# Optimization experiments

Hardware: AMD Instinct MI355X
Metric: run time of the kernel (lower is better)

The kernel has to match this reference:

```python
import jax, jax.numpy as jnp
import numpy as np

EMBED_DIM = 1024
PROJ_DIM = 256


def setup_inputs() -> dict:
    key = jax.random.key(0)
    kx, kq, kk = jax.random.split(key, 3)
    x = jax.random.normal(kx, (8, 4096, EMBED_DIM), dtype=jnp.float32)
    scale = 1.0 / (PROJ_DIM ** 0.5)
    q_proj = jax.random.normal(kq, (EMBED_DIM, PROJ_DIM), dtype=jnp.float32) * scale
    k_proj = jax.random.normal(kk, (EMBED_DIM, PROJ_DIM), dtype=jnp.float32) * scale
    return {"x": x, "q_proj": q_proj, "k_proj": k_proj}


def reference(x, q_proj, k_proj):
    # exp feature maps (FAVOR-style)
    q_prime = jnp.exp(jnp.einsum('bld,de->ble', x, q_proj))  # [B, L, E]
    k_prime = jnp.exp(jnp.einsum('bld,de->ble', x, k_proj))  # [B, L, E]
    # associative KV summary: O(L*E*D)
    kv = jnp.einsum('ble,bld->bed', k_prime, x)               # [B, E, D]
    num = jnp.einsum('ble,bed->bld', q_prime, kv)             # [B, L, D]
    z = 1.0 / (jnp.sum(q_prime, axis=-1, keepdims=True) + 1e-8)
    return num * z
```

## Files before the change

### kernel.cpp

```cpp
#include <hip/hip_runtime.h>


#define EMBED 1024
#define PROJ  256
#define LSEQ  4096
#define BATCH 8

typedef short  bfrag __attribute__((ext_vector_type(8)));
typedef float  f4    __attribute__((ext_vector_type(4)));
typedef unsigned short u16x8 __attribute__((ext_vector_type(8)));
typedef unsigned short u16x4 __attribute__((ext_vector_type(4)));

static __device__ __forceinline__ unsigned short f2bf(float f) {
  unsigned int u = __builtin_bit_cast(unsigned int, f);
  u += 0x7fffu + ((u >> 16) & 1u);
  return (unsigned short)(u >> 16);
}
static __device__ __forceinline__ float bf2f(unsigned short h) {
  unsigned int u = ((unsigned int)h) << 16;
  return __builtin_bit_cast(float, u);
}

static __device__ __forceinline__ void gload_lds16(const void* g, void* l) {
  __builtin_amdgcn_global_load_lds(
      (__attribute__((address_space(1))) void*)(unsigned long long)(g),
      (__attribute__((address_space(3))) void*)(unsigned)(unsigned long long)(l),
      16, 0, 0);
}

static __device__ __forceinline__ void stage_tile(
    const unsigned short* __restrict__ src, int row0, int stride, int k0,
    unsigned short* lds, int wave, int lane) {
#pragma unroll
  for (int j = 0; j < 4; j++) {
    int slot = (wave * 4 + j) * 64 + lane;
    int r = slot >> 3, cp = slot & 7;
    int c = cp ^ (r & 7);
    gload_lds16(src + (size_t)(row0 + r) * stride + k0 + c * 8,
                lds + (wave * 4 + j) * 512);
  }
}

static __device__ __forceinline__ bfrag read_frag(const unsigned short* lds,
                                                  int row, int chunk) {
  return *(const bfrag*)(lds + ((row << 3) + (chunk ^ (row & 7))) * 8);
}

__global__ __launch_bounds__(256) void cvtx_kernel(
    const float* __restrict__ x, unsigned short* __restrict__ xb,
    unsigned short* __restrict__ xT) {
  __shared__ unsigned short T[64][72];
  const int tid = threadIdx.x;
  const int d0 = blockIdx.x * 64, l0 = blockIdx.y * 64, b = blockIdx.z;
#pragma unroll
  for (int it = 0; it < 4; it++) {
    int slot = it * 256 + tid;
    int r = slot >> 4, c4 = slot & 15;
    f4 v = *(const f4*)(x + ((size_t)(b * LSEQ + l0 + r)) * EMBED + d0 + c4 * 4);
    u16x4 h = (u16x4){f2bf(v[0]), f2bf(v[1]), f2bf(v[2]), f2bf(v[3])};
    *(u16x4*)(xb + ((size_t)(b * LSEQ + l0 + r)) * EMBED + d0 + c4 * 4) = h;
    T[c4 * 4 + 0][r] = h[0];
    T[c4 * 4 + 1][r] = h[1];
    T[c4 * 4 + 2][r] = h[2];
    T[c4 * 4 + 3][r] = h[3];
  }
  __syncthreads();
#pragma unroll
  for (int it = 0; it < 2; it++) {
    int slot = it * 256 + tid;
    int d = slot >> 3, ch = slot & 7;
    *(u16x8*)(xT + ((size_t)(b * EMBED + d0 + d)) * LSEQ + l0 + ch * 8) =
        *(const u16x8*)&T[d][ch * 8];
  }
}

__global__ __launch_bounds__(256) void cvtw_kernel(
    const float* __restrict__ qw, const float* __restrict__ kw,
    unsigned short* __restrict__ wt) {
  __shared__ unsigned short T[64][72];
  const int tid = threadIdx.x;
  const int n0 = blockIdx.x * 64, k0 = blockIdx.y * 64;
  const float* W = blockIdx.z ? kw : qw;
#pragma unroll
  for (int it = 0; it < 4; it++) {
    int slot = it * 256 + tid;
    int r = slot >> 4, c4 = slot & 15;
    f4 v = *(const f4*)(W + (size_t)(k0 + r) * PROJ + n0 + c4 * 4);
#pragma unroll
    for (int j = 0; j < 4; j++) T[c4 * 4 + j][r] = f2bf(v[j]);
  }
  __syncthreads();
#pragma unroll
  for (int it = 0; it < 2; it++) {
    int slot = it * 256 + tid;
    int n = slot >> 3, ch = slot & 7;
    *(u16x8*)(wt + ((size_t)(blockIdx.z * PROJ + n0 + n)) * EMBED + k0 + ch * 8) =
        *(const u16x8*)&T[n][ch * 8];
  }
}

__global__ __launch_bounds__(256) void proj_kernel(
    const unsigned short* __restrict__ xb, const unsigned short* __restrict__ wt,
    unsigned short* __restrict__ qp, unsigned short* __restrict__ kT) {
  __shared__ union {
    struct { unsigned short A[128 * 64]; unsigned short B[128 * 64]; } t;
    unsigned short T[128 * 136];
  } sm;
  const int tid = threadIdx.x, wave = tid >> 6, lane = tid & 63;
  const int quad = lane >> 4, l16 = lane & 15;
  const int wm = wave >> 1, wn = wave & 1;
  const int n0 = blockIdx.x * 128, m0 = blockIdx.y * 128;

  f4 acc[4][4];
#pragma unroll
  for (int i = 0; i < 4; i++)
#pragma unroll
    for (int j = 0; j < 4; j++) acc[i][j] = (f4){0.f, 0.f, 0.f, 0.f};

  for (int k0 = 0; k0 < EMBED; k0 += 64) {
    stage_tile(xb, m0, EMBED, k0, sm.t.A, wave, lane);
    stage_tile(wt, n0, EMBED, k0, sm.t.B, wave, lane);
    __syncthreads();
#pragma unroll
    for (int ks = 0; ks < 2; ks++) {
      bfrag a[4], bfr[4];
#pragma unroll
      for (int mt = 0; mt < 4; mt++)
        a[mt] = read_frag(sm.t.A, wm * 64 + mt * 16 + l16, ks * 4 + quad);
#pragma unroll
      for (int nt = 0; nt < 4; nt++)
        bfr[nt] = read_frag(sm.t.B, wn * 64 + nt * 16 + l16, ks * 4 + quad);
#pragma unroll
      for (int mt = 0; mt < 4; mt++)
#pragma unroll
        for (int nt = 0; nt < 4; nt++)
          acc[mt][nt] = __builtin_amdgcn_mfma_f32_16x16x32_bf16(
              a[mt], bfr[nt], acc[mt][nt], 0, 0, 0);
    }
    __syncthreads();
  }

  if (n0 < PROJ) {
#pragma unroll
    for (int mt = 0; mt < 4; mt++)
#pragma unroll
      for (int nt = 0; nt < 4; nt++)
#pragma unroll
        for (int r = 0; r < 4; r++)
          sm.T[(wm * 64 + mt * 16 + quad * 4 + r) * 136 + wn * 64 + nt * 16 + l16] =
              f2bf(__expf(acc[mt][nt][r]));
    __syncthreads();
#pragma unroll
    for (int it = 0; it < 8; it++) {
      int slot = it * 256 + tid;
      int row = slot >> 4, ch = slot & 15;
      *(u16x8*)(qp + (size_t)(m0 + row) * PROJ + n0 + ch * 8) =
          *(const u16x8*)&sm.T[row * 136 + ch * 8];
    }
  } else {
#pragma unroll
    for (int mt = 0; mt < 4; mt++)
#pragma unroll
      for (int nt = 0; nt < 4; nt++) {
        u16x4 h;
#pragma unroll
        for (int r = 0; r < 4; r++) h[r] = f2bf(__expf(acc[mt][nt][r]));
        *(u16x4*)&sm.T[(wn * 64 + nt * 16 + l16) * 136 + wm * 64 + mt * 16 + quad * 4] = h;
      }
    __syncthreads();
    const int bb = m0 >> 12, l0 = m0 & 4095, ebase = n0 - PROJ;
#pragma unroll
    for (int it = 0; it < 8; it++) {
      int slot = it * 256 + tid;
      int e = slot >> 4, ch = slot & 15;
      *(u16x8*)(kT + (size_t)(bb * PROJ + ebase + e) * LSEQ + l0 + ch * 8) =
          *(const u16x8*)&sm.T[e * 136 + ch * 8];
    }
  }
}

__global__ __launch_bounds__(256) void zinv_kernel(
    const unsigned short* __restrict__ qp, float* __restrict__ zinv) {
  int m = blockIdx.x * 4 + (threadIdx.x >> 6);
  int lane = threadIdx.x & 63;
  u16x4 h = *(const u16x4*)(qp + (size_t)m * PROJ + lane * 4);
  float s = bf2f(h[0]) + bf2f(h[1]) + bf2f(h[2]) + bf2f(h[3]);
#pragma unroll
  for (int off = 32; off; off >>= 1) s += __shfl_xor(s, off);
  if (lane == 0) zinv[m] = 1.0f / (s + 1e-8f);
}

__global__ __launch_bounds__(256) void kv_kernel(
    const unsigned short* __restrict__ kT, const unsigned short* __restrict__ xT,
    float* __restrict__ kvp) {
  __shared__ struct { unsigned short A[128 * 64]; unsigned short B[128 * 64]; } sm;
  const int tid = threadIdx.x, wave = tid >> 6, lane = tid & 63;
  const int quad = lane >> 4, l16 = lane & 15;
  const int wm = wave >> 1, wn = wave & 1;
  const int d0 = blockIdx.x * 128, e0 = blockIdx.y * 128;
  const int b = blockIdx.z & 7, split = blockIdx.z >> 3;
  const unsigned short* As = kT + (size_t)b * PROJ * LSEQ;
  const unsigned short* Bs = xT + (size_t)b * EMBED * LSEQ;

  f4 acc[4][4];
#pragma unroll
  for (int i = 0; i < 4; i++)
#pragma unroll
    for (int j = 0; j < 4; j++) acc[i][j] = (f4){0.f, 0.f, 0.f, 0.f};

  const int kbase = split * 512;
  for (int kk = 0; kk < 512; kk += 64) {
    stage_tile(As, e0, LSEQ, kbase + kk, sm.A, wave, lane);
    stage_tile(Bs, d0, LSEQ, kbase + kk, sm.B, wave, lane);
    __syncthreads();
#pragma unroll
    for (int ks = 0; ks < 2; ks++) {
      bfrag a[4], bfr[4];
#pragma unroll
      for (int mt = 0; mt < 4; mt++)
        a[mt] = read_frag(sm.A, wm * 64 + mt * 16 + l16, ks * 4 + quad);
#pragma unroll
      for (int nt = 0; nt < 4; nt++)
        bfr[nt] = read_frag(sm.B, wn * 64 + nt * 16 + l16, ks * 4 + quad);
#pragma unroll
      for (int mt = 0; mt < 4; mt++)
#pragma unroll
        for (int nt = 0; nt < 4; nt++)
          acc[mt][nt] = __builtin_amdgcn_mfma_f32_16x16x32_bf16(
              a[mt], bfr[nt], acc[mt][nt], 0, 0, 0);
    }
    __syncthreads();
  }

#pragma unroll
  for (int mt = 0; mt < 4; mt++)
#pragma unroll
    for (int nt = 0; nt < 4; nt++)
#pragma unroll
      for (int r = 0; r < 4; r++) {
        int e = e0 + wm * 64 + mt * 16 + quad * 4 + r;
        int d = d0 + wn * 64 + nt * 16 + l16;
        kvp[((size_t)(split * 8 + b) * PROJ + e) * EMBED + d] = acc[mt][nt][r];
      }
}

__global__ __launch_bounds__(256) void kvreduce_kernel(
    const float* __restrict__ kvp, unsigned short* __restrict__ kvT) {
  __shared__ float T[64][68];
  const int tid = threadIdx.x;
  const int d0 = blockIdx.x * 64, e0 = blockIdx.y * 64, b = blockIdx.z;
#pragma unroll
  for (int it = 0; it < 4; it++) {
    int slot = it * 256 + tid;
    int e = slot >> 4, c4 = slot & 15;
    f4 s = (f4){0.f, 0.f, 0.f, 0.f};
#pragma unroll
    for (int sp = 0; sp < 8; sp++)
      s += *(const f4*)(kvp + ((size_t)(sp * 8 + b) * PROJ + e0 + e) * EMBED + d0 + c4 * 4);
#pragma unroll
    for (int j = 0; j < 4; j++) T[c4 * 4 + j][e] = s[j];
  }
  __syncthreads();
#pragma unroll
  for (int it = 0; it < 2; it++) {
    int slot = it * 256 + tid;
    int d = slot >> 3, ch = slot & 7;
    u16x8 h;
#pragma unroll
    for (int j = 0; j < 8; j++) h[j] = f2bf(T[d][ch * 8 + j]);
    *(u16x8*)(kvT + ((size_t)(b * EMBED + d0 + d)) * PROJ + e0 + ch * 8) = h;
  }
}

__global__ __launch_bounds__(256) void out_kernel(
    const unsigned short* __restrict__ qp, const unsigned short* __restrict__ kvT,
    const float* __restrict__ zinv, float* __restrict__ out) {
  __shared__ struct { unsigned short A[128 * 64]; unsigned short B[128 * 64]; } sm;
  __shared__ float zv[128];
  const int tid = threadIdx.x, wave = tid >> 6, lane = tid & 63;
  const int quad = lane >> 4, l16 = lane & 15;
  const int wm = wave >> 1, wn = wave & 1;
  const int d0 = blockIdx.x * 128, l0 = blockIdx.y * 128, b = blockIdx.z;
  const unsigned short* As = qp + (size_t)b * LSEQ * PROJ;
  const unsigned short* Bs = kvT + (size_t)b * EMBED * PROJ;

  if (tid < 128) zv[tid] = zinv[b * LSEQ + l0 + tid];

  f4 acc[4][4];
#pragma unroll
  for (int i = 0; i < 4; i++)
#pragma unroll
    for (int j = 0; j < 4; j++) acc[i][j] = (f4){0.f, 0.f, 0.f, 0.f};

  for (int k0 = 0; k0 < PROJ; k0 += 64) {
    stage_tile(As, l0, PROJ, k0, sm.A, wave, lane);
    stage_tile(Bs, d0, PROJ, k0, sm.B, wave, lane);
    __syncthreads();
#pragma unroll
    for (int ks = 0; ks < 2; ks++) {
      bfrag a[4], bfr[4];
#pragma unroll
      for (int mt = 0; mt < 4; mt++)
        a[mt] = read_frag(sm.A, wm * 64 + mt * 16 + l16, ks * 4 + quad);
#pragma unroll
      for (int nt = 0; nt < 4; nt++)
        bfr[nt] = read_frag(sm.B, wn * 64 + nt * 16 + l16, ks * 4 + quad);
#pragma unroll
      for (int mt = 0; mt < 4; mt++)
#pragma unroll
        for (int nt = 0; nt < 4; nt++)
          acc[mt][nt] = __builtin_amdgcn_mfma_f32_16x16x32_bf16(
              a[mt], bfr[nt], acc[mt][nt], 0, 0, 0);
    }
    __syncthreads();
  }

#pragma unroll
  for (int mt = 0; mt < 4; mt++)
#pragma unroll
    for (int nt = 0; nt < 4; nt++)
#pragma unroll
      for (int r = 0; r < 4; r++) {
        int row = wm * 64 + mt * 16 + quad * 4 + r;
        int d = d0 + wn * 64 + nt * 16 + l16;
        out[((size_t)(b * LSEQ + l0 + row)) * EMBED + d] = acc[mt][nt][r] * zv[row];
      }
}

extern "C" void kernel_launch(void* const* d_in, const int* in_sizes, int n_in,
                              void* d_out, int out_size, void* d_ws, size_t ws_size,
                              hipStream_t stream) {
  const float* x  = (const float*)d_in[0];
  const float* qw = (const float*)d_in[1];
  const float* kw = (const float*)d_in[2];
  float* out = (float*)d_out;

  char* ws = (char*)d_ws;
  unsigned short* xb   = (unsigned short*)(ws);
  unsigned short* xT   = (unsigned short*)(ws + 67108864);
  unsigned short* wt   = (unsigned short*)(ws + 134217728);
  unsigned short* qp   = (unsigned short*)(ws + 135266304);
  unsigned short* kT   = (unsigned short*)(ws + 152043520);
  unsigned short* kvT  = (unsigned short*)(ws + 168820736);
  float*          zinv = (float*)(ws + 173015040);
  float*          kvp  = (float*)(ws);

  cvtx_kernel<<<dim3(16, 64, 8), 256, 0, stream>>>(x, xb, xT);
  cvtw_kernel<<<dim3(4, 16, 2), 256, 0, stream>>>(qw, kw, wt);
  proj_kernel<<<dim3(4, 256), 256, 0, stream>>>(xb, wt, qp, kT);
  zinv_kernel<<<dim3(8192), 256, 0, stream>>>(qp, zinv);
  kv_kernel<<<dim3(8, 2, 64), 256, 0, stream>>>(kT, xT, kvp);
  kvreduce_kernel<<<dim3(16, 4, 8), 256, 0, stream>>>(kvp, kvT);
  out_kernel<<<dim3(8, 32, 8), 256, 0, stream>>>(qp, kvT, zinv, out);
}
```

Before: 396.3 us.

## Widen GEMM tiles, halve kv split-K, and transpose x in registers

The proj and out GEMMs move from 128x128 to 128x256 tiles. Each wave now holds a 4x8 accumulator grid, which raises reuse of the A tile but also raises register pressure. The kv split-K factor drops from 8 to 4, cutting partial-sum traffic and reduce work at the cost of fewer blocks. cvtx now transposes through registers instead of LDS. LDS padding also changes in cvtw and kvreduce.

```diff
diff --git a/kernel.cpp b/kernel.cpp
--- a/kernel.cpp
+++ b/kernel.cpp
@@ -28,16 +28,18 @@
       16, 0, 0);
 }
 
+template <int ROWS>
 static __device__ __forceinline__ void stage_tile(
     const unsigned short* __restrict__ src, int row0, int stride, int k0,
     unsigned short* lds, int wave, int lane) {
-#pragma unroll
-  for (int j = 0; j < 4; j++) {
-    int slot = (wave * 4 + j) * 64 + lane;
+  constexpr int G = ROWS / 32;
+#pragma unroll
+  for (int j = 0; j < G; j++) {
+    int slot = (wave * G + j) * 64 + lane;
     int r = slot >> 3, cp = slot & 7;
     int c = cp ^ (r & 7);
     gload_lds16(src + (size_t)(row0 + r) * stride + k0 + c * 8,
-                lds + (wave * 4 + j) * 512);
+                lds + (wave * G + j) * 512);
   }
 }
 
@@ -49,35 +51,32 @@
 __global__ __launch_bounds__(256) void cvtx_kernel(
     const float* __restrict__ x, unsigned short* __restrict__ xb,
     unsigned short* __restrict__ xT) {
-  __shared__ unsigned short T[64][72];
   const int tid = threadIdx.x;
-  const int d0 = blockIdx.x * 64, l0 = blockIdx.y * 64, b = blockIdx.z;
-#pragma unroll
-  for (int it = 0; it < 4; it++) {
-    int slot = it * 256 + tid;
-    int r = slot >> 4, c4 = slot & 15;
-    f4 v = *(const f4*)(x + ((size_t)(b * LSEQ + l0 + r)) * EMBED + d0 + c4 * 4);
-    u16x4 h = (u16x4){f2bf(v[0]), f2bf(v[1]), f2bf(v[2]), f2bf(v[3])};
-    *(u16x4*)(xb + ((size_t)(b * LSEQ + l0 + r)) * EMBED + d0 + c4 * 4) = h;
-    T[c4 * 4 + 0][r] = h[0];
-    T[c4 * 4 + 1][r] = h[1];
-    T[c4 * 4 + 2][r] = h[2];
-    T[c4 * 4 + 3][r] = h[3];
-  }
-  __syncthreads();
-#pragma unroll
-  for (int it = 0; it < 2; it++) {
-    int slot = it * 256 + tid;
-    int d = slot >> 3, ch = slot & 7;
-    *(u16x8*)(xT + ((size_t)(b * EMBED + d0 + d)) * LSEQ + l0 + ch * 8) =
-        *(const u16x8*)&T[d][ch * 8];
+  const int dc = tid & 15, lg = tid >> 4;
+  const int d0 = blockIdx.x * 64, l0 = blockIdx.y * 128, b = blockIdx.z;
+  const int l = l0 + lg * 8;
+  const int d = d0 + dc * 4;
+  unsigned short h[8][4];
+#pragma unroll
+  for (int j = 0; j < 8; j++) {
+    f4 v = *(const f4*)(x + ((size_t)(b * LSEQ + l + j)) * EMBED + d);
+    u16x4 hv = (u16x4){f2bf(v[0]), f2bf(v[1]), f2bf(v[2]), f2bf(v[3])};
+    *(u16x4*)(xb + ((size_t)(b * LSEQ + l + j)) * EMBED + d) = hv;
+    h[j][0] = hv[0]; h[j][1] = hv[1]; h[j][2] = hv[2]; h[j][3] = hv[3];
+  }
+#pragma unroll
+  for (int dd = 0; dd < 4; dd++) {
+    u16x8 t;
+#pragma unroll
+    for (int j = 0; j < 8; j++) t[j] = h[j][dd];
+    *(u16x8*)(xT + ((size_t)(b * EMBED + d + dd)) * LSEQ + l) = t;
   }
 }
 
 __global__ __launch_bounds__(256) void cvtw_kernel(
     const float* __restrict__ qw, const float* __restrict__ kw,
     unsigned short* __restrict__ wt) {
-  __shared__ unsigned short T[64][72];
+  __shared__ unsigned short T[64][66];
   const int tid = threadIdx.x;
   const int n0 = blockIdx.x * 64, k0 = blockIdx.y * 64;
   const float* W = blockIdx.z ? kw : qw;
@@ -103,78 +102,90 @@
     const unsigned short* __restrict__ xb, const unsigned short* __restrict__ wt,
     unsigned short* __restrict__ qp, unsigned short* __restrict__ kT) {
   __shared__ union {
-    struct { unsigned short A[128 * 64]; unsigned short B[128 * 64]; } t;
+    struct { unsigned short A[128 * 64]; unsigned short B[256 * 64]; } t;
     unsigned short T[128 * 136];
   } sm;
   const int tid = threadIdx.x, wave = tid >> 6, lane = tid & 63;
   const int quad = lane >> 4, l16 = lane & 15;
   const int wm = wave >> 1, wn = wave & 1;
-  const int n0 = blockIdx.x * 128, m0 = blockIdx.y * 128;
-
-  f4 acc[4][4];
+  const int n0 = blockIdx.x * 256, m0 = blockIdx.y * 128;
+
+  f4 acc[4][8];
 #pragma unroll
   for (int i = 0; i < 4; i++)
 #pragma unroll
-    for (int j = 0; j < 4; j++) acc[i][j] = (f4){0.f, 0.f, 0.f, 0.f};
+    for (int j = 0; j < 8; j++) acc[i][j] = (f4){0.f, 0.f, 0.f, 0.f};
 
   for (int k0 = 0; k0 < EMBED; k0 += 64) {
-    stage_tile(xb, m0, EMBED, k0, sm.t.A, wave, lane);
-    stage_tile(wt, n0, EMBED, k0, sm.t.B, wave, lane);
+    stage_tile<128>(xb, m0, EMBED, k0, sm.t.A, wave, lane);
+    stage_tile<256>(wt, n0, EMBED, k0, sm.t.B, wave, lane);
     __syncthreads();
 #pragma unroll
     for (int ks = 0; ks < 2; ks++) {
-      bfrag a[4], bfr[4];
+      bfrag a[4], bfr[8];
 #pragma unroll
       for (int mt = 0; mt < 4; mt++)
         a[mt] = read_frag(sm.t.A, wm * 64 + mt * 16 + l16, ks * 4 + quad);
 #pragma unroll
-      for (int nt = 0; nt < 4; nt++)
-        bfr[nt] = read_frag(sm.t.B, wn * 64 + nt * 16 + l16, ks * 4 + quad);
-#pragma unroll
-      for (int mt = 0; mt < 4; mt++)
-#pragma unroll
-        for (int nt = 0; nt < 4; nt++)
+      for (int nt = 0; nt < 8; nt++)
+        bfr[nt] = read_frag(sm.t.B, wn * 128 + nt * 16 + l16, ks * 4 + quad);
+#pragma unroll
+      for (int mt = 0; mt < 4; mt++)
+#pragma unroll
+        for (int nt = 0; nt < 8; nt++)
           acc[mt][nt] = __builtin_amdgcn_mfma_f32_16x16x32_bf16(
               a[mt], bfr[nt], acc[mt][nt], 0, 0, 0);
     }
     __syncthreads();
   }
 
-  if (n0 < PROJ) {
-#pragma unroll
-    for (int mt = 0; mt < 4; mt++)
-#pragma unroll
-      for (int nt = 0; nt < 4; nt++)
-#pragma unroll
-        for (int r = 0; r < 4; r++)
-          sm.T[(wm * 64 + mt * 16 + quad * 4 + r) * 136 + wn * 64 + nt * 16 + l16] =
-              f2bf(__expf(acc[mt][nt][r]));
-    __syncthreads();
-#pragma unroll
-    for (int it = 0; it < 8; it++) {
-      int slot = it * 256 + tid;
-      int row = slot >> 4, ch = slot & 15;
-      *(u16x8*)(qp + (size_t)(m0 + row) * PROJ + n0 + ch * 8) =
-          *(const u16x8*)&sm.T[row * 136 + ch * 8];
+  if (n0 == 0) {
+#pragma unroll
+    for (int h = 0; h < 2; h++) {
+      __syncthreads();
+      if (wn == h) {
+#pragma unroll
+        for (int mt = 0; mt < 4; mt++)
+#pragma unroll
+          for (int nt = 0; nt < 8; nt++)
+#pragma unroll
+            for (int r = 0; r < 4; r++)
+              sm.T[(wm * 64 + mt * 16 + quad * 4 + r) * 136 + nt * 16 + l16] =
+                  f2bf(__expf(acc[mt][nt][r]));
+      }
+      __syncthreads();
+#pragma unroll
+      for (int it = 0; it < 8; it++) {
+        int slot = it * 256 + tid;
+        int row = slot >> 4, ch = slot & 15;
+        *(u16x8*)(qp + (size_t)(m0 + row) * PROJ + h * 128 + ch * 8) =
+            *(const u16x8*)&sm.T[row * 136 + ch * 8];
+      }
     }
   } else {
-#pragma unroll
-    for (int mt = 0; mt < 4; mt++)
-#pragma unroll
-      for (int nt = 0; nt < 4; nt++) {
-        u16x4 h;
-#pragma unroll
-        for (int r = 0; r < 4; r++) h[r] = f2bf(__expf(acc[mt][nt][r]));
-        *(u16x4*)&sm.T[(wn * 64 + nt * 16 + l16) * 136 + wm * 64 + mt * 16 + quad * 4] = h;
-      }
-    __syncthreads();
-    const int bb = m0 >> 12, l0 = m0 & 4095, ebase = n0 - PROJ;
-#pragma unroll
-    for (int it = 0; it < 8; it++) {
-      int slot = it * 256 + tid;
-      int e = slot >> 4, ch = slot & 15;
-      *(u16x8*)(kT + (size_t)(bb * PROJ + ebase + e) * LSEQ + l0 + ch * 8) =
-          *(const u16x8*)&sm.T[e * 136 + ch * 8];
+    const int bb = m0 >> 12, ll0 = m0 & 4095;
+#pragma unroll
+    for (int h = 0; h < 2; h++) {
+      __syncthreads();
+      if (wn == h) {
+#pragma unroll
+        for (int mt = 0; mt < 4; mt++)
+#pragma unroll
+          for (int nt = 0; nt < 8; nt++) {
+            u16x4 hv;
+#pragma unroll
+            for (int r = 0; r < 4; r++) hv[r] = f2bf(__expf(acc[mt][nt][r]));
+            *(u16x4*)&sm.T[(nt * 16 + l16) * 136 + wm * 64 + mt * 16 + quad * 4] = hv;
+          }
+      }
+      __syncthreads();
+#pragma unroll
+      for (int it = 0; it < 8; it++) {
+        int slot = it * 256 + tid;
+        int e = slot >> 4, ch = slot & 15;
+        *(u16x8*)(kT + (size_t)(bb * PROJ + h * 128 + e) * LSEQ + ll0 + ch * 8) =
+            *(const u16x8*)&sm.T[e * 136 + ch * 8];
+      }
     }
   }
 }
@@ -208,10 +219,10 @@
 #pragma unroll
     for (int j = 0; j < 4; j++) acc[i][j] = (f4){0.f, 0.f, 0.f, 0.f};
 
-  const int kbase = split * 512;
-  for (int kk = 0; kk < 512; kk += 64) {
-    stage_tile(As, e0, LSEQ, kbase + kk, sm.A, wave, lane);
-    stage_tile(Bs, d0, LSEQ, kbase + kk, sm.B, wave, lane);
+  const int kbase = split * 1024;
+  for (int kk = 0; kk < 1024; kk += 64) {
+    stage_tile<128>(As, e0, LSEQ, kbase + kk, sm.A, wave, lane);
+    stage_tile<128>(Bs, d0, LSEQ, kbase + kk, sm.B, wave, lane);
     __syncthreads();
 #pragma unroll
     for (int ks = 0; ks < 2; ks++) {
@@ -246,7 +257,7 @@
 
 __global__ __launch_bounds__(256) void kvreduce_kernel(
     const float* __restrict__ kvp, unsigned short* __restrict__ kvT) {
-  __shared__ float T[64][68];
+  __shared__ float T[64][66];
   const int tid = threadIdx.x;
   const int d0 = blockIdx.x * 64, e0 = blockIdx.y * 64, b = blockIdx.z;
 #pragma unroll
@@ -255,7 +266,7 @@
     int e = slot >> 4, c4 = slot & 15;
     f4 s = (f4){0.f, 0.f, 0.f, 0.f};
 #pragma unroll
-    for (int sp = 0; sp < 8; sp++)
+    for (int sp = 0; sp < 4; sp++)
       s += *(const f4*)(kvp + ((size_t)(sp * 8 + b) * PROJ + e0 + e) * EMBED + d0 + c4 * 4);
 #pragma unroll
     for (int j = 0; j < 4; j++) T[c4 * 4 + j][e] = s[j];
@@ -275,40 +286,40 @@
 __global__ __launch_bounds__(256) void out_kernel(
     const unsigned short* __restrict__ qp, const unsigned short* __restrict__ kvT,
     const float* __restrict__ zinv, float* __restrict__ out) {
-  __shared__ struct { unsigned short A[128 * 64]; unsigned short B[128 * 64]; } sm;
+  __shared__ struct { unsigned short A[128 * 64]; unsigned short B[256 * 64]; } sm;
   __shared__ float zv[128];
   const int tid = threadIdx.x, wave = tid >> 6, lane = tid & 63;
   const int quad = lane >> 4, l16 = lane & 15;
   const int wm = wave >> 1, wn = wave & 1;
-  const int d0 = blockIdx.x * 128, l0 = blockIdx.y * 128, b = blockIdx.z;
+  const int d0 = blockIdx.x * 256, l0 = blockIdx.y * 128, b = blockIdx.z;
   const unsigned short* As = qp + (size_t)b * LSEQ * PROJ;
   const unsigned short* Bs = kvT + (size_t)b * EMBED * PROJ;
 
   if (tid < 128) zv[tid] = zinv[b * LSEQ + l0 + tid];
 
-  f4 acc[4][4];
+  f4 acc[4][8];
 #pragma unroll
   for (int i = 0; i < 4; i++)
 #pragma unroll
-    for (int j = 0; j < 4; j++) acc[i][j] = (f4){0.f, 0.f, 0.f, 0.f};
+    for (int j = 0; j < 8; j++) acc[i][j] = (f4){0.f, 0.f, 0.f, 0.f};
 
   for (int k0 = 0; k0 < PROJ; k0 += 64) {
-    stage_tile(As, l0, PROJ, k0, sm.A, wave, lane);
-    stage_tile(Bs, d0, PROJ, k0, sm.B, wave, lane);
+    stage_tile<128>(As, l0, PROJ, k0, sm.A, wave, lane);
+    stage_tile<256>(Bs, d0, PROJ, k0, sm.B, wave, lane);
     __syncthreads();
 #pragma unroll
     for (int ks = 0; ks < 2; ks++) {
-      bfrag a[4], bfr[4];
+      bfrag a[4], bfr[8];
 #pragma unroll
       for (int mt = 0; mt < 4; mt++)
         a[mt] = read_frag(sm.A, wm * 64 + mt * 16 + l16, ks * 4 + quad);
 #pragma unroll
-      for (int nt = 0; nt < 4; nt++)
-        bfr[nt] = read_frag(sm.B, wn * 64 + nt * 16 + l16, ks * 4 + quad);
-#pragma unroll
-      for (int mt = 0; mt < 4; mt++)
-#pragma unroll
-        for (int nt = 0; nt < 4; nt++)
+      for (int nt = 0; nt < 8; nt++)
+        bfr[nt] = read_frag(sm.B, wn * 128 + nt * 16 + l16, ks * 4 + quad);
+#pragma unroll
+      for (int mt = 0; mt < 4; mt++)
+#pragma unroll
+        for (int nt = 0; nt < 8; nt++)
           acc[mt][nt] = __builtin_amdgcn_mfma_f32_16x16x32_bf16(
               a[mt], bfr[nt], acc[mt][nt], 0, 0, 0);
     }
@@ -318,11 +329,11 @@
 #pragma unroll
   for (int mt = 0; mt < 4; mt++)
 #pragma unroll
-    for (int nt = 0; nt < 4; nt++)
+    for (int nt = 0; nt < 8; nt++)
 #pragma unroll
       for (int r = 0; r < 4; r++) {
         int row = wm * 64 + mt * 16 + quad * 4 + r;
-        int d = d0 + wn * 64 + nt * 16 + l16;
+        int d = d0 + wn * 128 + nt * 16 + l16;
         out[((size_t)(b * LSEQ + l0 + row)) * EMBED + d] = acc[mt][nt][r] * zv[row];
       }
 }
@@ -345,11 +356,11 @@
   float*          zinv = (float*)(ws + 173015040);
   float*          kvp  = (float*)(ws);
 
-  cvtx_kernel<<<dim3(16, 64, 8), 256, 0, stream>>>(x, xb, xT);
+  cvtx_kernel<<<dim3(16, 32, 8), 256, 0, stream>>>(x, xb, xT);
   cvtw_kernel<<<dim3(4, 16, 2), 256, 0, stream>>>(qw, kw, wt);
-  proj_kernel<<<dim3(4, 256), 256, 0, stream>>>(xb, wt, qp, kT);
+  proj_kernel<<<dim3(2, 256), 256, 0, stream>>>(xb, wt, qp, kT);
   zinv_kernel<<<dim3(8192), 256, 0, stream>>>(qp, zinv);
-  kv_kernel<<<dim3(8, 2, 64), 256, 0, stream>>>(kT, xT, kvp);
+  kv_kernel<<<dim3(8, 2, 32), 256, 0, stream>>>(kT, xT, kvp);
   kvreduce_kernel<<<dim3(16, 4, 8), 256, 0, stream>>>(kvp, kvT);
-  out_kernel<<<dim3(8, 32, 8), 256, 0, stream>>>(qp, kvT, zinv, out);
-}
+  out_kernel<<<dim3(4, 32, 8), 256, 0, stream>>>(qp, kvT, zinv, out);
+}
```

New measurement: 414.6 us. 1.05x slower.
